# Kernel tuning notes

Measured on AMD Instinct MI355X. Metric: run time of the kernel, lower is better.

## Reference

```python
import jax, jax.numpy as jnp
import numpy as np

INIT_RATIO = 0.5
TOT_EPOCHS = 100
TAU_A, TAU_B = 10.0, 0.1
MIN_NUM_C = 8
SEED = 777
SIGMA = 1.0
N, D = 3072, 128
E0 = 65536


def setup_inputs() -> dict:
    key = jax.random.key(0)
    k1, k2, k3, k4 = jax.random.split(key, 4)
    x = jax.random.normal(k1, (N, D), jnp.float32)
    edge_index = jax.random.randint(k2, (2, E0), 0, N, jnp.int32)
    score_w = jax.random.normal(k3, (1, D), jnp.float32)
    score_b = jnp.zeros((1,), jnp.float32)
    # scaled so per-edge attention logits stay in a sane softmax range
    att_params = jax.random.normal(k4, (2 * D, 1), jnp.float32) * 0.05
    return {"x": x, "edge_index": edge_index, "score_w": score_w,
            "score_b": score_b, "att_params": att_params, "epoch": 50}


def reference(x, edge_index, score_w, score_b, att_params, epoch):
    n, d = x.shape
    tau0 = TAU_A * (TAU_B / TAU_A) ** (epoch / TOT_EPOCHS)

    # ---- TopKPool scorer (single graph, batch = zeros) ----
    scores = (x @ score_w.T)[:, 0] + score_b[0]
    scores = scores / jnp.linalg.norm(score_w)
    k = int(np.ceil(INIT_RATIO * n))
    _, perm = jax.lax.top_k(scores, k)          # torch_geometric topk (desc)
    xk = x[perm]                                # [k, d]

    # ---- skip-edge construction: src i -> dest i+j, sliding windows ----
    fs = max(3, int(k / MIN_NUM_C))             # window size
    res = k - fs + 1                            # number of windows (rows)
    rows = jnp.repeat(jnp.arange(res), fs)      # dist_rowwise_inx, [E]
    offs = jnp.tile(jnp.arange(fs), res)        # dist_colwise_inx, [E]
    dests = rows + offs                         # node indices of window cols

    # ---- per-edge attention + scatter_softmax over rows ----
    wa = att_params[:d, 0]
    wb = att_params[d:, 0]
    sm = xk[rows] @ wa + xk[dests] @ wb                 # [E] == hstack @ att
    sm = jax.nn.softmax(sm.reshape(res, fs), axis=-1)   # uniform row size fs

    # ---- gaussian kernel over edge distances ----
    diff = xk[rows] - xk[dests]
    sq = jnp.sum(diff * diff, axis=-1)
    dist = jnp.sqrt(jnp.maximum(sq, 1e-24))             # safe L2 norm
    gk = jnp.exp(-dist / (2.0 * SIGMA ** 2)) - 1e-5
    gk = gk.reshape(res, fs)

    # ---- scatterSort: per-row stable descending sort, co-sort attention ----
    order = jnp.argsort(-gk, axis=-1)                   # stable by default
    gk_sort = jnp.take_along_axis(gk, order, axis=-1)
    sm_sort = jnp.take_along_axis(sm, order, axis=-1)

    # ---- column-wise logit aggregation + gumbel softmax ----
    logits_col = sm_sort.sum(axis=0)                    # scatter-sum over cols
    logits_all = jnp.broadcast_to(logits_col, (res, fs))
    one_mask = jnp.arange(fs) == 0                      # first slot of each row
    logits_all = jnp.where(one_mask, -jnp.inf, logits_all)
    g = jax.random.gumbel(jax.random.key(SEED), (res, fs), jnp.float32)
    gmb = jax.nn.softmax((g + logits_all) / tau0, axis=-1)

    logit_perrow = gk_sort * gmb                        # [res, fs]
    return logit_perrow.reshape(-1)
```

## Files before the change

### kernel.cpp

```cpp
#include <hip/hip_runtime.h>
#include <stdint.h>

#define N_T   3072
#define D_T   128
#define K_T   1536
#define FS_T  192
#define RES_T 1345
#define TOT_T (RES_T * FS_T)
#define TINYF 1.17549435e-38f
#define NBLK  256
#define NTHR  384
#define WPB   6
#define NWAVE (NBLK * WPB)
#define SLOT  32

__device__ __forceinline__ void ast_d(double* p, double v) { __hip_atomic_store(p, v, __ATOMIC_RELAXED, __HIP_MEMORY_SCOPE_AGENT); }
__device__ __forceinline__ void ast_f(float* p, float v)   { __hip_atomic_store(p, v, __ATOMIC_RELAXED, __HIP_MEMORY_SCOPE_AGENT); }
__device__ __forceinline__ void ast_i(int* p, int v)       { __hip_atomic_store(p, v, __ATOMIC_RELAXED, __HIP_MEMORY_SCOPE_AGENT); }
__device__ __forceinline__ double ald_d(double* p) { return __hip_atomic_load(p, __ATOMIC_RELAXED, __HIP_MEMORY_SCOPE_AGENT); }
__device__ __forceinline__ float  ald_f(float* p)  { return __hip_atomic_load(p, __ATOMIC_RELAXED, __HIP_MEMORY_SCOPE_AGENT); }
__device__ __forceinline__ int    ald_i(int* p)    { return __hip_atomic_load(p, __ATOMIC_RELAXED, __HIP_MEMORY_SCOPE_AGENT); }


__device__ __forceinline__ double wsumd(double v) {
  v += __shfl_xor(v, 1);  v += __shfl_xor(v, 2);  v += __shfl_xor(v, 4);
  v += __shfl_xor(v, 8);  v += __shfl_xor(v, 16); v += __shfl_xor(v, 32);
  return v;
}
__device__ __forceinline__ double wmaxd(double v) {
  v = fmax(v, __shfl_xor(v, 1));  v = fmax(v, __shfl_xor(v, 2));
  v = fmax(v, __shfl_xor(v, 4));  v = fmax(v, __shfl_xor(v, 8));
  v = fmax(v, __shfl_xor(v, 16)); v = fmax(v, __shfl_xor(v, 32));
  return v;
}
__device__ __forceinline__ float wsumf(float v) {
  v += __shfl_xor(v, 1);  v += __shfl_xor(v, 2);  v += __shfl_xor(v, 4);
  v += __shfl_xor(v, 8);  v += __shfl_xor(v, 16); v += __shfl_xor(v, 32);
  return v;
}
__device__ __forceinline__ float wmaxf(float v) {
  v = fmaxf(v, __shfl_xor(v, 1));  v = fmaxf(v, __shfl_xor(v, 2));
  v = fmaxf(v, __shfl_xor(v, 4));  v = fmaxf(v, __shfl_xor(v, 8));
  v = fmaxf(v, __shfl_xor(v, 16)); v = fmaxf(v, __shfl_xor(v, 32));
  return v;
}
__device__ __forceinline__ int wsumi(int v) {
  v += __shfl_xor(v, 1);  v += __shfl_xor(v, 2);  v += __shfl_xor(v, 4);
  v += __shfl_xor(v, 8);  v += __shfl_xor(v, 16); v += __shfl_xor(v, 32);
  return v;
}

#define ARR_SZ (4 * NBLK * SLOT)
__device__ __forceinline__ void grid_barrier(int* sync, int b) {
  asm volatile("s_waitcnt vmcnt(0)" ::: "memory");
  __syncthreads();
  int* arrive = sync + b * NBLK * SLOT;
  int* done   = sync + ARR_SZ + b * NBLK * SLOT;
  if (blockIdx.x == 0) {
    if (threadIdx.x < 64) {
      int lane = threadIdx.x;
      if (lane == 0) ast_i(&arrive[0], 1);
      for (;;) {
        int v0 = ald_i(&arrive[lane * SLOT]);
        int v1 = ald_i(&arrive[(lane + 64) * SLOT]);
        int v2 = ald_i(&arrive[(lane + 128) * SLOT]);
        int v3 = ald_i(&arrive[(lane + 192) * SLOT]);
        if (__all((v0 & v1 & v2 & v3) != 0)) break;
        __builtin_amdgcn_s_sleep(1);
      }
      ast_i(&done[lane * SLOT], 1);
      ast_i(&done[(lane + 64) * SLOT], 1);
      ast_i(&done[(lane + 128) * SLOT], 1);
      ast_i(&done[(lane + 192) * SLOT], 1);
    }
  } else {
    if (threadIdx.x == 0) {
      ast_i(&arrive[blockIdx.x * SLOT], 1);
      while (ald_i(&done[blockIdx.x * SLOT]) == 0) __builtin_amdgcn_s_sleep(2);
    }
  }
  asm volatile("" ::: "memory");
  __syncthreads();
}


__device__ __forceinline__ uint32_t rotl32(uint32_t x, uint32_t r) {
  return (x << r) | (x >> (32u - r));
}

__device__ __forceinline__ void threefry2x32(uint32_t k0, uint32_t k1,
                                             uint32_t x0, uint32_t x1,
                                             uint32_t& o0, uint32_t& o1) {
  uint32_t ks0 = k0, ks1 = k1, ks2 = k0 ^ k1 ^ 0x1BD11BDAu;
  x0 += ks0; x1 += ks1;
  x0 += x1; x1 = rotl32(x1, 13); x1 ^= x0;
  x0 += x1; x1 = rotl32(x1, 15); x1 ^= x0;
  x0 += x1; x1 = rotl32(x1, 26); x1 ^= x0;
  x0 += x1; x1 = rotl32(x1, 6);  x1 ^= x0;
  x0 += ks1; x1 += ks2 + 1u;
  x0 += x1; x1 = rotl32(x1, 17); x1 ^= x0;
  x0 += x1; x1 = rotl32(x1, 29); x1 ^= x0;
  x0 += x1; x1 = rotl32(x1, 16); x1 ^= x0;
  x0 += x1; x1 = rotl32(x1, 24); x1 ^= x0;
  x0 += ks2; x1 += ks0 + 2u;
  x0 += x1; x1 = rotl32(x1, 13); x1 ^= x0;
  x0 += x1; x1 = rotl32(x1, 15); x1 ^= x0;
  x0 += x1; x1 = rotl32(x1, 26); x1 ^= x0;
  x0 += x1; x1 = rotl32(x1, 6);  x1 ^= x0;
  x0 += ks0; x1 += ks1 + 3u;
  x0 += x1; x1 = rotl32(x1, 17); x1 ^= x0;
  x0 += x1; x1 = rotl32(x1, 29); x1 ^= x0;
  x0 += x1; x1 = rotl32(x1, 16); x1 ^= x0;
  x0 += x1; x1 = rotl32(x1, 24); x1 ^= x0;
  x0 += ks1; x1 += ks2 + 4u;
  x0 += x1; x1 = rotl32(x1, 13); x1 ^= x0;
  x0 += x1; x1 = rotl32(x1, 15); x1 ^= x0;
  x0 += x1; x1 = rotl32(x1, 26); x1 ^= x0;
  x0 += x1; x1 = rotl32(x1, 6);  x1 ^= x0;
  x0 += ks2; x1 += ks0 + 5u;
  o0 = x0; o1 = x1;
}

__device__ __forceinline__ float jax_gumbel(uint32_t i) {
  uint32_t o0, o1;
  threefry2x32(0u, 777u, 0u, i, o0, o1);
  uint32_t bits = o0 ^ o1;
  uint32_t fb = (bits >> 9) | 0x3F800000u;
  float u = __uint_as_float(fb) - 1.0f;
  float uu = fmaxf(TINYF, u + TINYF);
  return -logf(-logf(uu));
}

__global__ __launch_bounds__(NTHR, 2) void fused(
    const float* __restrict__ x, const float* __restrict__ sw,
    const float* __restrict__ att, const int* __restrict__ epoch_p,
    float* __restrict__ out, int* __restrict__ sync,
    double* __restrict__ scores, double* __restrict__ ball,
    double* __restrict__ logits, int* __restrict__ perm,
    float* __restrict__ sm_sort) {
  __shared__ double sc_lds[N_T];
  const int tid = threadIdx.x;
  const int lane = tid & 63;
  const int gw = blockIdx.x * WPB + (tid >> 6);

  for (int i = gw; i < N_T; i += NWAVE) {
    double xv0 = (double)x[i * D_T + lane];
    double xv1 = (double)x[i * D_T + 64 + lane];
    double ps = xv0 * (double)sw[lane] + xv1 * (double)sw[64 + lane];
    double pb = xv0 * (double)att[D_T + lane] + xv1 * (double)att[D_T + 64 + lane];
    ps = wsumd(ps);
    pb = wsumd(pb);
    if (lane == 0) { ast_d(&scores[i], ps); ast_d(&ball[i], pb); }
  }
  grid_barrier(sync, 0);

  for (int j = tid; j < N_T; j += NTHR) sc_lds[j] = ald_d(&scores[j]);
  __syncthreads();
  for (int i = gw; i < N_T; i += NWAVE) {
    double si = sc_lds[i];
    int cnt = 0;
#pragma unroll 8
    for (int j = lane; j < N_T; j += 64) {
      double sj = sc_lds[j];
      cnt += ((sj > si) || (sj == si && j < i)) ? 1 : 0;
    }
    cnt = wsumi(cnt);
    if (lane == 0 && cnt < K_T) ast_i(&perm[cnt], i);
  }
  grid_barrier(sync, 1);

  if (gw >= WPB && gw < WPB + RES_T) {
    int r = gw - WPB;
    int pr  = ald_i(&perm[r]);
    int pd0 = ald_i(&perm[r + lane]);
    int pd1 = ald_i(&perm[r + 64 + lane]);
    int pd2 = ald_i(&perm[r + 128 + lane]);

    double s0 = ald_d(&ball[pd0]), s1 = ald_d(&ball[pd1]), s2 = ald_d(&ball[pd2]);
    double mx = wmaxd(fmax(s0, fmax(s1, s2)));
    double e0 = exp(s0 - mx), e1 = exp(s1 - mx), e2 = exp(s2 - mx);
    double ssum = wsumd(e0 + e1 + e2);

    float xa = x[pr * D_T + lane];
    float xb = x[pr * D_T + 64 + lane];
    const float4* r0 = (const float4*)(x + (size_t)pd0 * D_T);
    const float4* r1 = (const float4*)(x + (size_t)pd1 * D_T);
    const float4* r2 = (const float4*)(x + (size_t)pd2 * D_T);
    double sq0 = 0.0, sq1 = 0.0, sq2 = 0.0;
#pragma unroll 4
    for (int tt = 0; tt < 32; ++tt) {
      float4 v0 = r0[tt], v1 = r1[tt], v2 = r2[tt];
      float src = (tt < 16) ? xa : xb;
      int base = (tt * 4) & 63;
      float u0 = __shfl(src, base);
      float u1 = __shfl(src, base + 1);
      float u2 = __shfl(src, base + 2);
      float u3 = __shfl(src, base + 3);
      float d;
      d = u0 - v0.x; sq0 += (double)d * (double)d;
      d = u1 - v0.y; sq0 += (double)d * (double)d;
      d = u2 - v0.z; sq0 += (double)d * (double)d;
      d = u3 - v0.w; sq0 += (double)d * (double)d;
      d = u0 - v1.x; sq1 += (double)d * (double)d;
      d = u1 - v1.y; sq1 += (double)d * (double)d;
      d = u2 - v1.z; sq1 += (double)d * (double)d;
      d = u3 - v1.w; sq1 += (double)d * (double)d;
      d = u0 - v2.x; sq2 += (double)d * (double)d;
      d = u1 - v2.y; sq2 += (double)d * (double)d;
      d = u2 - v2.z; sq2 += (double)d * (double)d;
      d = u3 - v2.w; sq2 += (double)d * (double)d;
    }
    double g0v = exp(-sqrt(fmax(sq0, 1e-24)) * 0.5) - 1e-5;
    double g1v = exp(-sqrt(fmax(sq1, 1e-24)) * 0.5) - 1e-5;
    double g2v = exp(-sqrt(fmax(sq2, 1e-24)) * 0.5) - 1e-5;

    int rk0 = 0, rk1 = 0, rk2 = 0;
#pragma unroll 4
    for (int j = 0; j < 64; ++j) {
      double h0 = __shfl(g0v, j), h1 = __shfl(g1v, j), h2 = __shfl(g2v, j);
      rk0 += ((h0 > g0v) || (h0 == g0v && j < lane)) ? 1 : 0;
      rk0 += (h1 > g0v) ? 1 : 0;
      rk0 += (h2 > g0v) ? 1 : 0;
      rk1 += ((h0 > g1v) || (h0 == g1v)) ? 1 : 0;
      rk1 += ((h1 > g1v) || (h1 == g1v && j < lane)) ? 1 : 0;
      rk1 += (h2 > g1v) ? 1 : 0;
      rk2 += ((h0 > g2v) || (h0 == g2v)) ? 1 : 0;
      rk2 += ((h1 > g2v) || (h1 == g2v)) ? 1 : 0;
      rk2 += ((h2 > g2v) || (h2 == g2v && j < lane)) ? 1 : 0;
    }
    size_t rb = (size_t)r * FS_T;
    double inv = 1.0 / ssum;
    ast_f(&out[rb + rk0], (float)g0v);  ast_f(&sm_sort[rb + rk0], (float)(e0 * inv));
    ast_f(&out[rb + rk1], (float)g1v);  ast_f(&sm_sort[rb + rk1], (float)(e1 * inv));
    ast_f(&out[rb + rk2], (float)g2v);  ast_f(&sm_sort[rb + rk2], (float)(e2 * inv));
  }
  grid_barrier(sync, 2);

  if (gw >= WPB && gw < WPB + FS_T) {
    int c = gw - WPB;
    double s = 0.0;
    for (int j = lane; j < RES_T; j += 64) s += (double)ald_f(&sm_sort[(size_t)j * FS_T + c]);
    s = wsumd(s);
    if (lane == 0) ast_d(&logits[c], s);
  }
  grid_barrier(sync, 3);

  if (gw < RES_T) {
    int r = gw;
    int i0 = r * FS_T + lane, i1 = i0 + 64, i2 = i0 + 128;
    float gk0 = ald_f(&out[i0]), gk1 = ald_f(&out[i1]), gk2 = ald_f(&out[i2]);
    float gb0 = jax_gumbel((uint32_t)i0);
    float gb1 = jax_gumbel((uint32_t)i1);
    float gb2 = jax_gumbel((uint32_t)i2);
    double l0 = ald_d(&logits[lane]);
    double l1 = ald_d(&logits[64 + lane]);
    double l2 = ald_d(&logits[128 + lane]);

    int ei = epoch_p[0];
    double epoch;
    if (ei >= 0 && ei <= 100000) epoch = (double)ei;
    else {
      float ef = __int_as_float(ei);
      epoch = (ef >= 0.0f && ef <= 100000.0f) ? (double)ef : 50.0;
    }
    double invtau = 0.1 * exp(0.04605170185988091 * epoch);

    float z0 = (lane == 0) ? -INFINITY : (float)(((double)gb0 + l0) * invtau);
    float z1 = (float)(((double)gb1 + l1) * invtau);
    float z2 = (float)(((double)gb2 + l2) * invtau);
    float m = wmaxf(fmaxf(z0, fmaxf(z1, z2)));
    float e0 = (lane == 0) ? 0.0f : expf(z0 - m);
    float e1 = expf(z1 - m);
    float e2 = expf(z2 - m);
    float ssum = wsumf(e0 + e1 + e2);
    float invs = 1.0f / ssum;
    out[i0] = gk0 * (e0 * invs);
    out[i1] = gk1 * (e1 * invs);
    out[i2] = gk2 * (e2 * invs);
  }
}

extern "C" void kernel_launch(void* const* d_in, const int* in_sizes, int n_in,
                              void* d_out, int out_size, void* d_ws, size_t ws_size,
                              hipStream_t stream) {
  const float* x   = (const float*)d_in[0];
  const float* sw  = (const float*)d_in[2];
  const float* att = (const float*)d_in[4];
  const int* epoch = (const int*)d_in[5];
  float* out = (float*)d_out;

  char* ws = (char*)d_ws;
  size_t sync_bytes = (size_t)2 * ARR_SZ * sizeof(int);
  int*    sync    = (int*)ws;
  double* scores  = (double*)(ws + sync_bytes);
  double* ball    = scores + N_T;
  double* logits  = ball + N_T;
  int*    perm    = (int*)(logits + FS_T);
  float*  sm_sort = (float*)(perm + K_T);

  (void)hipMemsetAsync(sync, 0, sync_bytes, stream);
  fused<<<NBLK, NTHR, 0, stream>>>(x, sw, att, epoch, out, sync,
                                   scores, ball, logits, perm, sm_sort);
}
```

Measured before the change: 64.48 us.

## Fuse column logit reduction into attention stage via LDS and atomics

```diff
diff --git a/kernel.cpp b/kernel.cpp
--- a/kernel.cpp
+++ b/kernel.cpp
@@ -9,10 +9,11 @@
 #define TOT_T (RES_T * FS_T)
 #define TINYF 1.17549435e-38f
 #define NBLK  256
-#define NTHR  384
-#define WPB   6
+#define NTHR  1024
+#define WPB   16
 #define NWAVE (NBLK * WPB)
 #define SLOT  32
+#define ARR_SZ (4 * NBLK * SLOT)
 
 __device__ __forceinline__ void ast_d(double* p, double v) { __hip_atomic_store(p, v, __ATOMIC_RELAXED, __HIP_MEMORY_SCOPE_AGENT); }
 __device__ __forceinline__ void ast_f(float* p, float v)   { __hip_atomic_store(p, v, __ATOMIC_RELAXED, __HIP_MEMORY_SCOPE_AGENT); }
@@ -50,7 +51,6 @@
   return v;
 }
 
-#define ARR_SZ (4 * NBLK * SLOT)
 __device__ __forceinline__ void grid_barrier(int* sync, int b) {
   asm volatile("s_waitcnt vmcnt(0)" ::: "memory");
   __syncthreads();
@@ -131,19 +131,20 @@
   return -logf(-logf(uu));
 }
 
-__global__ __launch_bounds__(NTHR, 2) void fused(
+__global__ __launch_bounds__(NTHR, 4) void fused(
     const float* __restrict__ x, const float* __restrict__ sw,
     const float* __restrict__ att, const int* __restrict__ epoch_p,
     float* __restrict__ out, int* __restrict__ sync,
-    double* __restrict__ scores, double* __restrict__ ball,
-    double* __restrict__ logits, int* __restrict__ perm,
-    float* __restrict__ sm_sort) {
-  __shared__ double sc_lds[N_T];
+    double* __restrict__ logits, double* __restrict__ scores,
+    double* __restrict__ ball, int* __restrict__ perm) {
+  __shared__ double lds64[N_T];
   const int tid = threadIdx.x;
   const int lane = tid & 63;
-  const int gw = blockIdx.x * WPB + (tid >> 6);
-
-  for (int i = gw; i < N_T; i += NWAVE) {
+  const int w = tid >> 6;
+  const int gw = blockIdx.x * WPB + w;
+
+  if (gw < N_T) {
+    int i = gw;
     double xv0 = (double)x[i * D_T + lane];
     double xv1 = (double)x[i * D_T + 64 + lane];
     double ps = xv0 * (double)sw[lane] + xv1 * (double)sw[64 + lane];
@@ -154,14 +155,20 @@
   }
   grid_barrier(sync, 0);
 
-  for (int j = tid; j < N_T; j += NTHR) sc_lds[j] = ald_d(&scores[j]);
+  {
+    double s0 = ald_d(&scores[tid]);
+    double s1 = ald_d(&scores[tid + NTHR]);
+    double s2 = ald_d(&scores[tid + 2 * NTHR]);
+    lds64[tid] = s0; lds64[tid + NTHR] = s1; lds64[tid + 2 * NTHR] = s2;
+  }
   __syncthreads();
-  for (int i = gw; i < N_T; i += NWAVE) {
-    double si = sc_lds[i];
+  if (gw < N_T) {
+    int i = gw;
+    double si = lds64[i];
     int cnt = 0;
 #pragma unroll 8
     for (int j = lane; j < N_T; j += 64) {
-      double sj = sc_lds[j];
+      double sj = lds64[j];
       cnt += ((sj > si) || (sj == si && j < i)) ? 1 : 0;
     }
     cnt = wsumi(cnt);
@@ -169,82 +176,92 @@
   }
   grid_barrier(sync, 1);
 
-  if (gw >= WPB && gw < WPB + RES_T) {
-    int r = gw - WPB;
-    int pr  = ald_i(&perm[r]);
-    int pd0 = ald_i(&perm[r + lane]);
-    int pd1 = ald_i(&perm[r + 64 + lane]);
-    int pd2 = ald_i(&perm[r + 128 + lane]);
-
-    double s0 = ald_d(&ball[pd0]), s1 = ald_d(&ball[pd1]), s2 = ald_d(&ball[pd2]);
-    double mx = wmaxd(fmax(s0, fmax(s1, s2)));
-    double e0 = exp(s0 - mx), e1 = exp(s1 - mx), e2 = exp(s2 - mx);
-    double ssum = wsumd(e0 + e1 + e2);
-
-    float xa = x[pr * D_T + lane];
-    float xb = x[pr * D_T + 64 + lane];
-    const float4* r0 = (const float4*)(x + (size_t)pd0 * D_T);
-    const float4* r1 = (const float4*)(x + (size_t)pd1 * D_T);
-    const float4* r2 = (const float4*)(x + (size_t)pd2 * D_T);
-    double sq0 = 0.0, sq1 = 0.0, sq2 = 0.0;
+  {
+    const bool blockHasRows = (blockIdx.x * WPB) < RES_T;
+    if (blockHasRows) {
+      for (int j = tid; j < WPB * FS_T; j += NTHR) lds64[j] = 0.0;
+      __syncthreads();
+      if (gw < RES_T) {
+        int r = gw;
+        int pr  = ald_i(&perm[r]);
+        int pd0 = ald_i(&perm[r + lane]);
+        int pd1 = ald_i(&perm[r + 64 + lane]);
+        int pd2 = ald_i(&perm[r + 128 + lane]);
+
+        double s0 = ald_d(&ball[pd0]), s1 = ald_d(&ball[pd1]), s2 = ald_d(&ball[pd2]);
+        double mx = wmaxd(fmax(s0, fmax(s1, s2)));
+        double e0 = exp(s0 - mx), e1 = exp(s1 - mx), e2 = exp(s2 - mx);
+        double ssum = wsumd(e0 + e1 + e2);
+
+        float xa = x[pr * D_T + lane];
+        float xb = x[pr * D_T + 64 + lane];
+        const float4* r0 = (const float4*)(x + (size_t)pd0 * D_T);
+        const float4* r1 = (const float4*)(x + (size_t)pd1 * D_T);
+        const float4* r2 = (const float4*)(x + (size_t)pd2 * D_T);
+        double sq0 = 0.0, sq1 = 0.0, sq2 = 0.0;
 #pragma unroll 4
-    for (int tt = 0; tt < 32; ++tt) {
-      float4 v0 = r0[tt], v1 = r1[tt], v2 = r2[tt];
-      float src = (tt < 16) ? xa : xb;
-      int base = (tt * 4) & 63;
-      float u0 = __shfl(src, base);
-      float u1 = __shfl(src, base + 1);
-      float u2 = __shfl(src, base + 2);
-      float u3 = __shfl(src, base + 3);
-      float d;
-      d = u0 - v0.x; sq0 += (double)d * (double)d;
-      d = u1 - v0.y; sq0 += (double)d * (double)d;
-      d = u2 - v0.z; sq0 += (double)d * (double)d;
-      d = u3 - v0.w; sq0 += (double)d * (double)d;
-      d = u0 - v1.x; sq1 += (double)d * (double)d;
-      d = u1 - v1.y; sq1 += (double)d * (double)d;
-      d = u2 - v1.z; sq1 += (double)d * (double)d;
-      d = u3 - v1.w; sq1 += (double)d * (double)d;
-      d = u0 - v2.x; sq2 += (double)d * (double)d;
-      d = u1 - v2.y; sq2 += (double)d * (double)d;
-      d = u2 - v2.z; sq2 += (double)d * (double)d;
-      d = u3 - v2.w; sq2 += (double)d * (double)d;
-    }
-    double g0v = exp(-sqrt(fmax(sq0, 1e-24)) * 0.5) - 1e-5;
-    double g1v = exp(-sqrt(fmax(sq1, 1e-24)) * 0.5) - 1e-5;
-    double g2v = exp(-sqrt(fmax(sq2, 1e-24)) * 0.5) - 1e-5;
-
-    int rk0 = 0, rk1 = 0, rk2 = 0;
+        for (int tt = 0; tt < 32; ++tt) {
+          float4 v0 = r0[tt], v1 = r1[tt], v2 = r2[tt];
+          float src = (tt < 16) ? xa : xb;
+          int base = (tt * 4) & 63;
+          float u0 = __shfl(src, base);
+          float u1 = __shfl(src, base + 1);
+          float u2 = __shfl(src, base + 2);
+          float u3 = __shfl(src, base + 3);
+          float d;
+          d = u0 - v0.x; sq0 += (double)d * (double)d;
+          d = u1 - v0.y; sq0 += (double)d * (double)d;
+          d = u2 - v0.z; sq0 += (double)d * (double)d;
+          d = u3 - v0.w; sq0 += (double)d * (double)d;
+          d = u0 - v1.x; sq1 += (double)d * (double)d;
+          d = u1 - v1.y; sq1 += (double)d * (double)d;
+          d = u2 - v1.z; sq1 += (double)d * (double)d;
+          d = u3 - v1.w; sq1 += (double)d * (double)d;
+          d = u0 - v2.x; sq2 += (double)d * (double)d;
+          d = u1 - v2.y; sq2 += (double)d * (double)d;
+          d = u2 - v2.z; sq2 += (double)d * (double)d;
+          d = u3 - v2.w; sq2 += (double)d * (double)d;
+        }
+        double g0v = exp(-sqrt(fmax(sq0, 1e-24)) * 0.5) - 1e-5;
+        double g1v = exp(-sqrt(fmax(sq1, 1e-24)) * 0.5) - 1e-5;
+        double g2v = exp(-sqrt(fmax(sq2, 1e-24)) * 0.5) - 1e-5;
+
+        int rk0 = 0, rk1 = 0, rk2 = 0;
 #pragma unroll 4
-    for (int j = 0; j < 64; ++j) {
-      double h0 = __shfl(g0v, j), h1 = __shfl(g1v, j), h2 = __shfl(g2v, j);
-      rk0 += ((h0 > g0v) || (h0 == g0v && j < lane)) ? 1 : 0;
-      rk0 += (h1 > g0v) ? 1 : 0;
-      rk0 += (h2 > g0v) ? 1 : 0;
-      rk1 += ((h0 > g1v) || (h0 == g1v)) ? 1 : 0;
-      rk1 += ((h1 > g1v) || (h1 == g1v && j < lane)) ? 1 : 0;
-      rk1 += (h2 > g1v) ? 1 : 0;
-      rk2 += ((h0 > g2v) || (h0 == g2v)) ? 1 : 0;
-      rk2 += ((h1 > g2v) || (h1 == g2v)) ? 1 : 0;
-      rk2 += ((h2 > g2v) || (h2 == g2v && j < lane)) ? 1 : 0;
-    }
-    size_t rb = (size_t)r * FS_T;
-    double inv = 1.0 / ssum;
-    ast_f(&out[rb + rk0], (float)g0v);  ast_f(&sm_sort[rb + rk0], (float)(e0 * inv));
-    ast_f(&out[rb + rk1], (float)g1v);  ast_f(&sm_sort[rb + rk1], (float)(e1 * inv));
-    ast_f(&out[rb + rk2], (float)g2v);  ast_f(&sm_sort[rb + rk2], (float)(e2 * inv));
+        for (int j = 0; j < 64; ++j) {
+          double h0 = __shfl(g0v, j), h1 = __shfl(g1v, j), h2 = __shfl(g2v, j);
+          rk0 += ((h0 > g0v) || (h0 == g0v && j < lane)) ? 1 : 0;
+          rk0 += (h1 > g0v) ? 1 : 0;
+          rk0 += (h2 > g0v) ? 1 : 0;
+          rk1 += ((h0 > g1v) || (h0 == g1v)) ? 1 : 0;
+          rk1 += ((h1 > g1v) || (h1 == g1v && j < lane)) ? 1 : 0;
+          rk1 += (h2 > g1v) ? 1 : 0;
+          rk2 += ((h0 > g2v) || (h0 == g2v)) ? 1 : 0;
+          rk2 += ((h1 > g2v) || (h1 == g2v)) ? 1 : 0;
+          rk2 += ((h2 > g2v) || (h2 == g2v && j < lane)) ? 1 : 0;
+        }
+        size_t rb = (size_t)r * FS_T;
+        double inv = 1.0 / ssum;
+        ast_f(&out[rb + rk0], (float)g0v);
+        ast_f(&out[rb + rk1], (float)g1v);
+        ast_f(&out[rb + rk2], (float)g2v);
+        lds64[w * FS_T + rk0] = e0 * inv;
+        lds64[w * FS_T + rk1] = e1 * inv;
+        lds64[w * FS_T + rk2] = e2 * inv;
+      }
+      __syncthreads();
+      if (tid < FS_T) {
+        double s = 0.0;
+#pragma unroll
+        for (int k = 0; k < WPB; ++k) s += lds64[k * FS_T + tid];
+        atomicAdd(&logits[tid], s);
+      }
+    }
   }
   grid_barrier(sync, 2);
 
-  if (gw >= WPB && gw < WPB + FS_T) {
-    int c = gw - WPB;
-    double s = 0.0;
-    for (int j = lane; j < RES_T; j += 64) s += (double)ald_f(&sm_sort[(size_t)j * FS_T + c]);
-    s = wsumd(s);
-    if (lane == 0) ast_d(&logits[c], s);
-  }
-  grid_barrier(sync, 3);
-
+  if (tid < FS_T) lds64[tid] = ald_d(&logits[tid]);
+  __syncthreads();
   if (gw < RES_T) {
     int r = gw;
     int i0 = r * FS_T + lane, i1 = i0 + 64, i2 = i0 + 128;
@@ -252,9 +269,7 @@
     float gb0 = jax_gumbel((uint32_t)i0);
     float gb1 = jax_gumbel((uint32_t)i1);
     float gb2 = jax_gumbel((uint32_t)i2);
-    double l0 = ald_d(&logits[lane]);
-    double l1 = ald_d(&logits[64 + lane]);
-    double l2 = ald_d(&logits[128 + lane]);
+    double l0 = lds64[lane], l1 = lds64[64 + lane], l2 = lds64[128 + lane];
 
     int ei = epoch_p[0];
     double epoch;
@@ -290,15 +305,14 @@
   float* out = (float*)d_out;
 
   char* ws = (char*)d_ws;
-  size_t sync_bytes = (size_t)2 * ARR_SZ * sizeof(int);
+  const size_t sync_bytes = (size_t)2 * ARR_SZ * sizeof(int);
   int*    sync    = (int*)ws;
-  double* scores  = (double*)(ws + sync_bytes);
+  double* logits  = (double*)(ws + sync_bytes);
+  double* scores  = logits + 256;
   double* ball    = scores + N_T;
-  double* logits  = ball + N_T;
-  int*    perm    = (int*)(logits + FS_T);
-  float*  sm_sort = (float*)(perm + K_T);
-
-  (void)hipMemsetAsync(sync, 0, sync_bytes, stream);
+  int*    perm    = (int*)(ball + N_T);
+
+  (void)hipMemsetAsync(sync, 0, sync_bytes + 256 * sizeof(double), stream);
   fused<<<NBLK, NTHR, 0, stream>>>(x, sw, att, epoch, out, sync,
-                                   scores, ball, logits, perm, sm_sort);
-}
+                                   logits, scores, ball, perm);
+}
```

New measurement: 78.41 us. 21.6% more time.
